# Performance work log

Measured on AMD Instinct MI355X. Metric: run time of the kernel, lower is better.

Reference implementation:

```python
import jax, jax.numpy as jnp
import numpy as np

E, H, T_MAX = 1024, 16, 2048
HS = E // H
EPS = 1e-5


def _layernorm(x, g, b):
    m = jnp.mean(x, axis=-1, keepdims=True)
    v = jnp.mean(jnp.square(x - m), axis=-1, keepdims=True)
    return (x - m) * jax.lax.rsqrt(v + EPS) * g + b


def setup_inputs() -> dict:
    key = jax.random.key(0)
    ks = jax.random.split(key, 8)
    B, T = 2, 2048
    s = 0.02
    return {
        "x": jax.random.normal(ks[0], (B, T, E), jnp.float32),
        "ln1_g": jnp.ones((E,), jnp.float32),
        "ln1_b": jnp.zeros((E,), jnp.float32),
        "Wk": jax.random.normal(ks[1], (H, E, HS), jnp.float32) * s,  # stacked per-head key weights (x @ Wk)
        "Wv": jax.random.normal(ks[2], (H, E, HS), jnp.float32) * s,
        "Wproj": jax.random.normal(ks[3], (E, E), jnp.float32) * s,
        "bproj": jnp.zeros((E,), jnp.float32),
        "ln2_g": jnp.ones((E,), jnp.float32),
        "ln2_b": jnp.zeros((E,), jnp.float32),
        "W1": jax.random.normal(ks[4], (E, 4 * E), jnp.float32) * s,
        "b1": jnp.zeros((4 * E,), jnp.float32),
        "W2": jax.random.normal(ks[5], (4 * E, E), jnp.float32) * s,
        "b2": jnp.zeros((E,), jnp.float32),
    }


def reference(x, ln1_g, ln1_b, Wk, Wv, Wproj, bproj, ln2_g, ln2_b, W1, b1, W2, b2):
    B, T, C = x.shape
    h = _layernorm(x, ln1_g, ln1_b)
    # NOTE: original code uses the KEY projection for both q and k (q = self.key(x))
    k = jnp.einsum('bte,hed->bhtd', h, Wk)
    q = k
    wei = jnp.einsum('bhtd,bhsd->bhts', q, k) * (C ** -0.5)  # scale by full n_embd, as in source
    causal = jnp.tril(jnp.ones((T, T), bool))
    wei = jnp.where(causal, wei, -jnp.inf)
    # source applies softmax over dim=1 (the query/row axis of the TxT matrix)
    wei = jax.nn.softmax(wei, axis=2)
    v = jnp.einsum('bte,hed->bhtd', h, Wv)
    attn = jnp.einsum('bhts,bhsd->bhtd', wei, v)          # [B,H,T,HS]
    attn = attn.transpose(0, 2, 1, 3).reshape(B, T, C)    # concat heads
    x = x + attn @ Wproj + bproj
    h2 = _layernorm(x, ln2_g, ln2_b)
    x = x + jax.nn.relu(h2 @ W1 + b1) @ W2 + b2
    return x
```

## Files before the change

kernel.cpp:

```cpp
#include <hip/hip_runtime.h>

using bf16x8 = __attribute__((ext_vector_type(8))) __bf16;
using f32x4  = __attribute__((ext_vector_type(4))) float;

__device__ __forceinline__ f32x4 mfma16(bf16x8 a, bf16x8 b, f32x4 c) {
  return __builtin_amdgcn_mfma_f32_16x16x32_bf16(a, b, c, 0, 0, 0);
}

__device__ __forceinline__ unsigned short f2bf(float f) {
  union { float f; unsigned int u; } x; x.f = f;
  unsigned int u = x.u + 0x7FFFu + ((x.u >> 16) & 1u);
  return (unsigned short)(u >> 16);
}

__device__ __forceinline__ unsigned int cvtpk_bf16(float lo, float hi) {
  unsigned int r;
  asm("v_cvt_pk_bf16_f32 %0, %1, %2" : "=v"(r) : "v"(lo), "v"(hi));
  return r;
}

__device__ __forceinline__ float fexp2(float x) {
#if __has_builtin(__builtin_amdgcn_exp2f)
  return __builtin_amdgcn_exp2f(x);
#else
  float r; asm("v_exp_f32 %0, %1" : "=v"(r) : "v"(x)); return r;
#endif
}

__device__ __forceinline__ void gl_lds16(const unsigned short* g, unsigned short* l) {
  __builtin_amdgcn_global_load_lds(
      (__attribute__((address_space(1))) void*)(g),
      (__attribute__((address_space(3))) void*)(l), 16, 0, 0);
}

__device__ __forceinline__ bf16x8 rdsw64(const unsigned short* base, int r, int ch) {
  int c = ch ^ (r & 7);
  return *reinterpret_cast<const bf16x8*>(base + ((size_t)r * 8 + c) * 8);
}

__global__ __launch_bounds__(256) void transpose_cvt(const float* __restrict__ in,
                                                     unsigned short* __restrict__ out,
                                                     int R, int C) {
  __shared__ float t[32][33];
  int b = blockIdx.z;
  const float* inb = in + (size_t)b * R * C;
  unsigned short* outb = out + (size_t)b * R * C;
  int tx = threadIdx.x & 31, ty = threadIdx.x >> 5;
  int c0 = blockIdx.x * 32, r0 = blockIdx.y * 32;
#pragma unroll
  for (int i = 0; i < 4; ++i)
    t[ty + i * 8][tx] = inb[(size_t)(r0 + ty + i * 8) * C + c0 + tx];
  __syncthreads();
#pragma unroll
  for (int i = 0; i < 4; ++i)
    outb[(size_t)(c0 + ty + i * 8) * R + r0 + tx] = f2bf(t[tx][ty + i * 8]);
}

__global__ __launch_bounds__(256) void ln_bf16(const float* __restrict__ x,
                                               const float* __restrict__ g,
                                               const float* __restrict__ bta,
                                               unsigned short* __restrict__ out) {
  int row = blockIdx.x, tid = threadIdx.x;
  float4 v = reinterpret_cast<const float4*>(x + (size_t)row * 1024)[tid];
  float s = v.x + v.y + v.z + v.w;
  float s2 = v.x * v.x + v.y * v.y + v.z * v.z + v.w * v.w;
#pragma unroll
  for (int m = 1; m < 64; m <<= 1) { s += __shfl_xor(s, m); s2 += __shfl_xor(s2, m); }
  __shared__ float red[8];
  int w = tid >> 6;
  if ((tid & 63) == 0) { red[w] = s; red[w + 4] = s2; }
  __syncthreads();
  s  = red[0] + red[1] + red[2] + red[3];
  s2 = red[4] + red[5] + red[6] + red[7];
  float mean = s * (1.f / 1024.f);
  float var  = s2 * (1.f / 1024.f) - mean * mean;
  float rstd = rsqrtf(var + 1e-5f);
  float4 gv = reinterpret_cast<const float4*>(g)[tid];
  float4 bv = reinterpret_cast<const float4*>(bta)[tid];
  ushort4 o;
  o.x = f2bf((v.x - mean) * rstd * gv.x + bv.x);
  o.y = f2bf((v.y - mean) * rstd * gv.y + bv.y);
  o.z = f2bf((v.z - mean) * rstd * gv.z + bv.z);
  o.w = f2bf((v.w - mean) * rstd * gv.w + bv.w);
  reinterpret_cast<ushort4*>(out + (size_t)row * 1024)[tid] = o;
}

__device__ __forceinline__ void stage_half(const unsigned short* gbase, int K,
                                           unsigned short* lds, int tid) {
#pragma unroll
  for (int j = 0; j < 2; ++j) {
    int lr = j * 64 + (tid >> 3);
    int c  = (tid & 7) ^ (lr & 7);
    gl_lds16(gbase + (size_t)lr * K + c * 8, lds + (size_t)(j * 512 + tid) * 8);
  }
}

__device__ __forceinline__ bf16x8 rdfrag(const unsigned short* base, int r, int k) {
  return *reinterpret_cast<const bf16x8*>(base + ((size_t)r * 8 + (k ^ (r & 7))) * 8);
}

__global__ __launch_bounds__(512, 2) void gemm256_relu(const unsigned short* __restrict__ A,
                                                       const unsigned short* __restrict__ Bt,
                                                       unsigned short* __restrict__ C,
                                                       const float* __restrict__ bias,
                                                       int M, int N, int K) {
  __shared__ __align__(16) unsigned short LA[2][256 * 64];
  __shared__ __align__(16) unsigned short LB[2][256 * 64];
  int tid = threadIdx.x, lane = tid & 63, w = tid >> 6;
  int l15 = lane & 15, lh = lane >> 4;
  int wr = (w >> 2) * 128, wc = (w & 3) * 64;
  int bid = blockIdx.x;
  int xcd = bid & 7, g = bid >> 3;
  int bm = (xcd >> 1) * 4 + (g >> 3);
  int bn = (xcd & 1) * 8 + (g & 7);
  const unsigned short* Ab = A + (size_t)(bm * 256) * K;
  const unsigned short* Bb = Bt + (size_t)(bn * 256) * K;
  f32x4 acc[8][4] = {};
  int NT = K >> 6;
  stage_half(Ab, K, &LA[0][0], tid);
  stage_half(Ab + (size_t)128 * K, K, &LA[0][128 * 64], tid);
  stage_half(Bb, K, &LB[0][0], tid);
  stage_half(Bb + (size_t)128 * K, K, &LB[0][128 * 64], tid);
  asm volatile("s_waitcnt vmcnt(0)" ::: "memory");
  __builtin_amdgcn_s_barrier();
  for (int t = 0; t < NT; ++t) {
    int cur = t & 1;
    const unsigned short* la = &LA[cur][0];
    const unsigned short* lb = &LB[cur][0];
    unsigned short* na = &LA[cur ^ 1][0];
    unsigned short* nb = &LB[cur ^ 1][0];
    int k0n = (t + 1) << 6;
    bool more = (t + 1 < NT);
    bf16x8 bfr[4][2];
#pragma unroll
    for (int q = 0; q < 4; ++q) {
      if (more) {
        if (q == 0)      stage_half(Ab + k0n, K, na, tid);
        else if (q == 1) stage_half(Ab + (size_t)128 * K + k0n, K, na + 128 * 64, tid);
        else if (q == 2) stage_half(Bb + k0n, K, nb, tid);
        else             stage_half(Bb + (size_t)128 * K + k0n, K, nb + 128 * 64, tid);
      }
      if (q == 0) {
        if (more) asm volatile("s_waitcnt vmcnt(2)" ::: "memory");
        else      asm volatile("s_waitcnt vmcnt(0)" ::: "memory");
        __builtin_amdgcn_s_barrier();
      }
      bf16x8 aq[2][2];
#pragma unroll
      for (int i = 0; i < 2; ++i)
#pragma unroll
        for (int kk = 0; kk < 2; ++kk)
          aq[i][kk] = rdfrag(la, wr + q * 32 + i * 16 + l15, kk * 4 + lh);
      if (q == 0) {
#pragma unroll
        for (int ni = 0; ni < 4; ++ni)
#pragma unroll
          for (int kk = 0; kk < 2; ++kk)
            bfr[ni][kk] = rdfrag(lb, wc + ni * 16 + l15, kk * 4 + lh);
      }
      if (q != 0) __builtin_amdgcn_s_barrier();
      __builtin_amdgcn_s_setprio(1);
#pragma unroll
      for (int kk = 0; kk < 2; ++kk)
#pragma unroll
        for (int i = 0; i < 2; ++i)
#pragma unroll
          for (int ni = 0; ni < 4; ++ni)
            acc[q * 2 + i][ni] = mfma16(aq[i][kk], bfr[ni][kk], acc[q * 2 + i][ni]);
      __builtin_amdgcn_s_setprio(0);
      __builtin_amdgcn_s_barrier();
    }
  }
#pragma unroll
  for (int mi = 0; mi < 8; ++mi)
#pragma unroll
    for (int ni = 0; ni < 4; ++ni) {
      int row0 = bm * 256 + wr + mi * 16 + lh * 4;
      int col  = bn * 256 + wc + ni * 16 + l15;
      float bv = bias[col];
#pragma unroll
      for (int r = 0; r < 4; ++r) {
        float v = fmaxf(acc[mi][ni][r] + bv, 0.f);
        C[(size_t)(row0 + r) * N + col] = f2bf(v);
      }
    }
}

#define GBK 128
#define KSCL 0.04508422f

__device__ __forceinline__ bf16x8 rd128(const unsigned short* base, int r, int ch) {
  int c = ch ^ ((r & 7) << 1);
  return *reinterpret_cast<const bf16x8*>(base + (size_t)r * GBK + c * 8);
}

template<int TM, int MODE>
__global__ __launch_bounds__(256) void gemm_bf16(const unsigned short* __restrict__ A,
                                                 const unsigned short* __restrict__ Bt,
                                                 void* __restrict__ Cout,
                                                 unsigned short* __restrict__ Cout2,
                                                 const float* __restrict__ bias,
                                                 const float* __restrict__ resid,
                                                 const float* __restrict__ scvec,
                                                 int M, int N, int K) {
  constexpr int MI = TM / 32;
  constexpr int AJ = TM / 16;
  __shared__ __align__(16) unsigned short Sh[(TM + 128) * GBK];
  unsigned short* As = Sh;
  unsigned short* Bs = Sh + TM * GBK;
  int tid = threadIdx.x;
  int lane = tid & 63, w = tid >> 6;
  int l15 = lane & 15, lh = lane >> 4;
  int wr = (w >> 1) * (TM / 2), wc = (w & 1) * 64;
  int nblk = N >> 7;
  int rows = M / TM;
  int bm, bn;
  if (nblk == 8 && (rows & 7) == 0) {
    int bid = blockIdx.x;
    int xcd = bid & 7, g = bid >> 3;
    bm = xcd * (rows >> 3) + (g >> 3);
    bn = g & 7;
  } else {
    bm = blockIdx.x / nblk; bn = blockIdx.x % nblk;
  }
  const unsigned short* ApJ[AJ];
  const unsigned short* BpJ[8];
#pragma unroll
  for (int j = 0; j < AJ; ++j) {
    int row = j * 16 + (tid >> 4);
    int ch  = (tid & 15) ^ ((row & 7) << 1);
    ApJ[j] = A + (size_t)(bm * TM + row) * K + ch * 8;
  }
#pragma unroll
  for (int j = 0; j < 8; ++j) {
    int row = j * 16 + (tid >> 4);
    int ch  = (tid & 15) ^ ((row & 7) << 1);
    BpJ[j] = Bt + (size_t)(bn * 128 + row) * K + ch * 8;
  }
  f32x4 acc[MI][4] = {};
  for (int k0 = 0; k0 < K; k0 += GBK) {
#pragma unroll
    for (int j = 0; j < AJ; ++j)
      gl_lds16(ApJ[j] + k0, &As[(j * 256 + tid) * 8]);
#pragma unroll
    for (int j = 0; j < 8; ++j)
      gl_lds16(BpJ[j] + k0, &Bs[(j * 256 + tid) * 8]);
    __syncthreads();
    bf16x8 af[MI][4], bfr[4][4];
#pragma unroll
    for (int i = 0; i < MI; ++i)
#pragma unroll
      for (int kk = 0; kk < 4; ++kk)
        af[i][kk] = rd128(As, wr + i * 16 + l15, kk * 4 + lh);
#pragma unroll
    for (int i = 0; i < 4; ++i)
#pragma unroll
      for (int kk = 0; kk < 4; ++kk)
        bfr[i][kk] = rd128(Bs, wc + i * 16 + l15, kk * 4 + lh);
#pragma unroll
    for (int kk = 0; kk < 4; ++kk)
#pragma unroll
      for (int mi = 0; mi < MI; ++mi)
#pragma unroll
        for (int ni = 0; ni < 4; ++ni)
          acc[mi][ni] = mfma16(af[mi][kk], bfr[ni][kk], acc[mi][ni]);
    __syncthreads();
  }
  if constexpr (MODE == 3) {
#pragma unroll
    for (int mi = 0; mi < MI; ++mi) {
#pragma unroll
      for (int ni = 0; ni < 4; ++ni) {
        int tl = wr + mi * 16 + lh * 4;
        int dl = wc + ni * 16 + l15;
        int colg = bn * 128 + dl;
        int bb = bm >> 5, hh = colg >> 6;
        const float* sp = scvec + (size_t)(bb * 16 + hh) * 2048 + (bm & 31) * 64 + tl;
        float4 rs = *reinterpret_cast<const float4*>(sp);
        unsigned int p0 = f2bf(acc[mi][ni][0] * rs.x) | ((unsigned int)f2bf(acc[mi][ni][1] * rs.y) << 16);
        unsigned int p1 = f2bf(acc[mi][ni][2] * rs.z) | ((unsigned int)f2bf(acc[mi][ni][3] * rs.w) << 16);
        uint2 pk = {p0, p1};
        *reinterpret_cast<uint2*>(&Sh[dl * 64 + (tl ^ ((dl & 7) << 3))]) = pk;
      }
    }
    __syncthreads();
    int dr = tid >> 1, th = (tid & 1) * 32;
    int bb = bm >> 5, tbase = (bm & 31) * 64;
    size_t colg = bn * 128 + dr;
    unsigned short* Vt = (unsigned short*)Cout;
#pragma unroll
    for (int j = 0; j < 4; ++j) {
      int t = th + j * 8;
      int4 v = *reinterpret_cast<const int4*>(&Sh[dr * 64 + (t ^ ((dr & 7) << 3))]);
      *reinterpret_cast<int4*>(&Vt[((size_t)bb * 1024 + colg) * 2048 + tbase + t]) = v;
    }
  } else {
#pragma unroll
    for (int mi = 0; mi < MI; ++mi) {
#pragma unroll
      for (int ni = 0; ni < 4; ++ni) {
        int row0 = bm * TM + wr + mi * 16 + lh * 4;
        int col  = bn * 128 + wc + ni * 16 + l15;
        float bv = (MODE == 2) ? 0.f : bias[col];
#pragma unroll
        for (int r = 0; r < 4; ++r) {
          int row = row0 + r;
          float v = acc[mi][ni][r] + bv;
          if constexpr (MODE == 0) {
            v += resid[(size_t)row * N + col];
            ((float*)Cout)[(size_t)row * N + col] = v;
          } else {
            ((unsigned short*)Cout)[(size_t)row * N + col] = f2bf(v);
            Cout2[(size_t)row * N + col] = f2bf(v * KSCL);
          }
        }
      }
    }
  }
}

__global__ __launch_bounds__(512) void attn_stats(const unsigned short* __restrict__ Kb,
                                                  const unsigned short* __restrict__ Kbs,
                                                  float* __restrict__ colrcp) {
  __shared__ __align__(16) unsigned short Kt[2][64 * 64];
  int bid = blockIdx.x;
  int q = bid >> 8, x = (bid >> 5) & 7, bh = bid & 31;
  int b = bh >> 4, h = bh & 15;
  int sb = q ? (15 - x) : x;
  int tid = threadIdx.x, lane = tid & 63, w = tid >> 6;
  int l15 = lane & 15, lh = lane >> 4;
  int s0 = sb * 128, sw = s0 + w * 16;
  const unsigned short* Kp  = Kb  + ((size_t)b * 2048) * 1024 + h * 64;
  const unsigned short* Kps = Kbs + ((size_t)b * 2048) * 1024 + h * 64;
  bf16x8 as[2];
#pragma unroll
  for (int kc = 0; kc < 2; ++kc)
    as[kc] = *reinterpret_cast<const bf16x8*>(Kp + (size_t)(sw + l15) * 1024 + kc * 32 + (lh << 3));
  int srow = tid >> 3;
  int sch  = (tid & 7) ^ (srow & 7);
  const unsigned short* ksrc = Kps + (size_t)srow * 1024 + sch * 8;
  gl_lds16(ksrc + (size_t)s0 * 1024, &Kt[0][tid * 8]);
  __syncthreads();
  float l[4] = {0.f, 0.f, 0.f, 0.f};
  int nt = 32 - 2 * sb;
  for (int it = 0; it < nt; ++it) {
    int t0 = s0 + it * 64;
    int cur = it & 1;
    if (it + 1 < nt)
      gl_lds16(ksrc + (size_t)(t0 + 64) * 1024, &Kt[cur ^ 1][tid * 8]);
    if (t0 + 63 >= sw) {
      bool dmask = (t0 < sw + 16);
#pragma unroll
      for (int tf = 0; tf < 4; ++tf) {
        int tr = tf * 16 + l15;
        bf16x8 bt0 = rdsw64(&Kt[cur][0], tr, lh);
        bf16x8 bt1 = rdsw64(&Kt[cur][0], tr, 4 + lh);
        f32x4 z = {};
        f32x4 sa = mfma16(as[1], bt1, mfma16(as[0], bt0, z));
        int tg = t0 + tr;
#pragma unroll
        for (int r = 0; r < 4; ++r) {
          float e = fexp2(sa[r]);
          if (dmask) { int sg = sw + lh * 4 + r; e = (tg >= sg) ? e : 0.f; }
          l[r] += e;
        }
      }
    }
    __syncthreads();
  }
#pragma unroll
  for (int m = 1; m < 16; m <<= 1)
#pragma unroll
    for (int r = 0; r < 4; ++r)
      l[r] += __shfl_xor(l[r], m);
  if (l15 == 0) {
#pragma unroll
    for (int r = 0; r < 4; ++r)
      colrcp[(size_t)bh * 2048 + sw + lh * 4 + r] = 1.f / l[r];
  }
}

__global__ __launch_bounds__(512) void attn_pv(const unsigned short* __restrict__ Kb,
                                               const unsigned short* __restrict__ Kbs,
                                               const unsigned short* __restrict__ Vt,
                                               unsigned short* __restrict__ attn) {
  __shared__ __align__(16) unsigned short Ks[2][64 * 64];
  __shared__ __align__(16) unsigned short Vs[3][64 * 64];
  __shared__ __align__(16) unsigned short Pl[8][2][16][68];
  int bid = blockIdx.x;
  int q = bid >> 8, x = (bid >> 5) & 7, bh = bid & 31;
  int b = bh >> 4, h = bh & 15;
  int tb = q ? x : (15 - x);
  int tid = threadIdx.x, lane = tid & 63, w = tid >> 6;
  int l15 = lane & 15, lh = lane >> 4;
  int t0 = tb * 128, tw = t0 + w * 16;
  const unsigned short* Kp  = Kb  + ((size_t)b * 2048) * 1024 + h * 64;
  const unsigned short* Kps = Kbs + ((size_t)b * 2048) * 1024 + h * 64;
  const unsigned short* Vp  = Vt + (size_t)bh * 64 * 2048;
  bf16x8 at[2];
#pragma unroll
  for (int kc = 0; kc < 2; ++kc)
    at[kc] = *reinterpret_cast<const bf16x8*>(Kp + (size_t)(tw + l15) * 1024 + kc * 32 + (lh << 3));
  int srow = tid >> 3;
  int sch  = (tid & 7) ^ (srow & 7);
  const unsigned short* ksrc = Kps + (size_t)srow * 1024 + sch * 8;
  const unsigned short* vsrc = Vp + (size_t)srow * 2048 + sch * 8;
  int nt = 2 * tb + 2;
  gl_lds16(ksrc, &Ks[0][tid * 8]);
  gl_lds16(vsrc, &Vs[0][tid * 8]);
  __syncthreads();
  f32x4 acc[4] = {};
  for (int it = 0; it < nt; ++it) {
    int s0 = it * 64;
    const unsigned short* ksCur = &Ks[it & 1][0];
    if (it + 1 < nt) {
      gl_lds16(ksrc + (size_t)(s0 + 64) * 1024, &Ks[(it + 1) & 1][tid * 8]);
      gl_lds16(vsrc + (s0 + 64), &Vs[(it + 1) % 3][tid * 8]);
    }
    if (s0 <= tw + 15) {
      bool dmask = (s0 + 63 > tw);
#pragma unroll
      for (int sf = 0; sf < 4; ++sf) {
        int sr = sf * 16 + l15;
        bf16x8 ks0 = rdsw64(ksCur, sr, lh);
        bf16x8 ks1 = rdsw64(ksCur, sr, 4 + lh);
        f32x4 z = {};
        f32x4 sa = mfma16(ks1, at[1], mfma16(ks0, at[0], z));
        float pe[4];
#pragma unroll
        for (int r = 0; r < 4; ++r) {
          float p = fexp2(sa[r]);
          if (dmask) {
            int sg = s0 + sf * 16 + lh * 4 + r;
            int tg = tw + l15;
            p = (sg <= tg) ? p : 0.f;
          }
          pe[r] = p;
        }
        unsigned int u0 = cvtpk_bf16(pe[0], pe[1]);
        unsigned int u1 = cvtpk_bf16(pe[2], pe[3]);
        unsigned long long pk = (unsigned long long)u0 | ((unsigned long long)u1 << 32);
        *reinterpret_cast<unsigned long long*>(&Pl[w][it & 1][l15][sf * 16 + lh * 4]) = pk;
      }
    }
    if (it > 0) {
      int pit = it - 1;
      if (pit * 64 <= tw + 15) {
        const unsigned short* vsPrev = &Vs[pit % 3][0];
#pragma unroll
        for (int c2 = 0; c2 < 2; ++c2) {
          bf16x8 pa = *reinterpret_cast<const bf16x8*>(&Pl[w][pit & 1][l15][c2 * 32 + (lh << 3)]);
#pragma unroll
          for (int nf = 0; nf < 4; ++nf) {
            int dr = nf * 16 + l15;
            bf16x8 vb = rdsw64(vsPrev, dr, c2 * 4 + lh);
            acc[nf] = mfma16(pa, vb, acc[nf]);
          }
        }
      }
    }
    __syncthreads();
  }
  {
    int pit = nt - 1;
    if (pit * 64 <= tw + 15) {
      const unsigned short* vsPrev = &Vs[pit % 3][0];
#pragma unroll
      for (int c2 = 0; c2 < 2; ++c2) {
        bf16x8 pa = *reinterpret_cast<const bf16x8*>(&Pl[w][pit & 1][l15][c2 * 32 + (lh << 3)]);
#pragma unroll
        for (int nf = 0; nf < 4; ++nf) {
          int dr = nf * 16 + l15;
          bf16x8 vb = rdsw64(vsPrev, dr, c2 * 4 + lh);
          acc[nf] = mfma16(pa, vb, acc[nf]);
        }
      }
    }
  }
#pragma unroll
  for (int nf = 0; nf < 4; ++nf)
#pragma unroll
    for (int r = 0; r < 4; ++r) {
      int t = tw + lh * 4 + r;
      attn[(size_t)(b * 2048 + t) * 1024 + h * 64 + nf * 16 + l15] = f2bf(acc[nf][r]);
    }
}

extern "C" void kernel_launch(void* const* d_in, const int* in_sizes, int n_in,
                              void* d_out, int out_size, void* d_ws, size_t ws_size,
                              hipStream_t stream) {
  (void)in_sizes; (void)n_in; (void)out_size; (void)ws_size;
  const float* x     = (const float*)d_in[0];
  const float* ln1_g = (const float*)d_in[1];
  const float* ln1_b = (const float*)d_in[2];
  const float* Wk    = (const float*)d_in[3];
  const float* Wv    = (const float*)d_in[4];
  const float* Wproj = (const float*)d_in[5];
  const float* bproj = (const float*)d_in[6];
  const float* ln2_g = (const float*)d_in[7];
  const float* ln2_b = (const float*)d_in[8];
  const float* W1    = (const float*)d_in[9];
  const float* b1    = (const float*)d_in[10];
  const float* W2    = (const float*)d_in[11];
  const float* b2    = (const float*)d_in[12];
  float* out = (float*)d_out;

  char* ws = (char*)d_ws;
  size_t off = 0;
  auto alloc = [&](size_t bytes) { void* p = ws + off; off += (bytes + 255) & ~(size_t)255; return p; };
  unsigned short* bufA = (unsigned short*)alloc((size_t)4096 * 1024 * 2);
  unsigned short* wk_t = (unsigned short*)alloc((size_t)1024 * 1024 * 2);
  unsigned short* wv_t = (unsigned short*)alloc((size_t)1024 * 1024 * 2);
  unsigned short* wp_t = (unsigned short*)alloc((size_t)1024 * 1024 * 2);
  unsigned short* w1_t = (unsigned short*)alloc((size_t)1024 * 4096 * 2);
  unsigned short* w2_t = (unsigned short*)alloc((size_t)4096 * 1024 * 2);
  unsigned short* Kb   = (unsigned short*)alloc((size_t)4096 * 1024 * 2);
  unsigned short* Kbs  = (unsigned short*)alloc((size_t)4096 * 1024 * 2);
  unsigned short* Vt   = (unsigned short*)alloc((size_t)4096 * 1024 * 2);
  float* colrcp = (float*)alloc((size_t)32 * 2048 * 4);
  float* y      = (float*)alloc((size_t)4096 * 1024 * 4);
  unsigned short* act = (unsigned short*)alloc((size_t)4096 * 4096 * 2);

  dim3 b256(256), b512(512);
  transpose_cvt<<<dim3(2, 32, 16), b256, 0, stream>>>(Wk, wk_t, 1024, 64);
  transpose_cvt<<<dim3(2, 32, 16), b256, 0, stream>>>(Wv, wv_t, 1024, 64);
  transpose_cvt<<<dim3(32, 32, 1), b256, 0, stream>>>(Wproj, wp_t, 1024, 1024);
  transpose_cvt<<<dim3(128, 32, 1), b256, 0, stream>>>(W1, w1_t, 1024, 4096);
  transpose_cvt<<<dim3(32, 128, 1), b256, 0, stream>>>(W2, w2_t, 4096, 1024);

  ln_bf16<<<4096, b256, 0, stream>>>(x, ln1_g, ln1_b, bufA);
  gemm_bf16<64, 2><<<512, b256, 0, stream>>>(bufA, wk_t, Kb, Kbs, nullptr, nullptr, nullptr, 4096, 1024, 1024);
  attn_stats<<<512, b512, 0, stream>>>(Kb, Kbs, colrcp);
  gemm_bf16<64, 3><<<512, b256, 0, stream>>>(bufA, wv_t, Vt, nullptr, nullptr, nullptr, colrcp, 4096, 1024, 1024);
  attn_pv<<<512, b512, 0, stream>>>(Kb, Kbs, Vt, bufA);
  gemm_bf16<64, 0><<<512, b256, 0, stream>>>(bufA, wp_t, y, nullptr, bproj, x, nullptr, 4096, 1024, 1024);
  ln_bf16<<<4096, b256, 0, stream>>>(y, ln2_g, ln2_b, bufA);
  gemm256_relu<<<256, dim3(512), 0, stream>>>(bufA, w1_t, act, b1, 4096, 4096, 1024);
  gemm_bf16<64, 0><<<512, b256, 0, stream>>>(act, w2_t, out, nullptr, b2, y, nullptr, 4096, 1024, 4096);
}
```

Baseline: 240.1 us.

## Double-buffer LDS in generic bf16 GEMM with BK=64 and prefetch overlap

The generic bf16 GEMM moves from a single-buffered K-tile of 128 to two LDS buffers of K=64. Loads for the next tile are issued before the MFMAs on the current tile, and a partial vmcnt wait plus raw barriers replace the full __syncthreads. The goal is to hide global-to-LDS latency behind compute. The change also raises wave priority around the MFMA block. In exchange there are twice as many loop iterations and barriers, and the kernel relies on an rdsw64 helper that is assumed to exist elsewhere.

```diff
diff --git a/kernel.cpp b/kernel.cpp
--- a/kernel.cpp
+++ b/kernel.cpp
@@ -186,13 +186,7 @@
     }
 }
 
-#define GBK 128
 #define KSCL 0.04508422f
-
-__device__ __forceinline__ bf16x8 rd128(const unsigned short* base, int r, int ch) {
-  int c = ch ^ ((r & 7) << 1);
-  return *reinterpret_cast<const bf16x8*>(base + (size_t)r * GBK + c * 8);
-}
 
 template<int TM, int MODE>
 __global__ __launch_bounds__(256) void gemm_bf16(const unsigned short* __restrict__ A,
@@ -203,11 +197,10 @@
                                                  const float* __restrict__ resid,
                                                  const float* __restrict__ scvec,
                                                  int M, int N, int K) {
-  constexpr int MI = TM / 32;
-  constexpr int AJ = TM / 16;
-  __shared__ __align__(16) unsigned short Sh[(TM + 128) * GBK];
-  unsigned short* As = Sh;
-  unsigned short* Bs = Sh + TM * GBK;
+  constexpr int MI  = TM / 32;
+  constexpr int ALD = TM / 32;
+  constexpr int NLD = ALD + 4;
+  __shared__ __align__(16) unsigned short Sh[2][(TM + 128) * 64];
   int tid = threadIdx.x;
   int lane = tid & 63, w = tid >> 6;
   int l15 = lane & 15, lh = lane >> 4;
@@ -223,49 +216,68 @@
   } else {
     bm = blockIdx.x / nblk; bn = blockIdx.x % nblk;
   }
-  const unsigned short* ApJ[AJ];
-  const unsigned short* BpJ[8];
-#pragma unroll
-  for (int j = 0; j < AJ; ++j) {
-    int row = j * 16 + (tid >> 4);
-    int ch  = (tid & 15) ^ ((row & 7) << 1);
-    ApJ[j] = A + (size_t)(bm * TM + row) * K + ch * 8;
-  }
-#pragma unroll
-  for (int j = 0; j < 8; ++j) {
-    int row = j * 16 + (tid >> 4);
-    int ch  = (tid & 15) ^ ((row & 7) << 1);
-    BpJ[j] = Bt + (size_t)(bn * 128 + row) * K + ch * 8;
+  const unsigned short* Asrc[ALD];
+  const unsigned short* Bsrc[4];
+#pragma unroll
+  for (int j = 0; j < ALD; ++j) {
+    int row = j * 32 + (tid >> 3);
+    int ch  = (tid & 7) ^ (row & 7);
+    Asrc[j] = A + (size_t)(bm * TM + row) * K + ch * 8;
+  }
+#pragma unroll
+  for (int j = 0; j < 4; ++j) {
+    int row = j * 32 + (tid >> 3);
+    int ch  = (tid & 7) ^ (row & 7);
+    Bsrc[j] = Bt + (size_t)(bn * 128 + row) * K + ch * 8;
   }
   f32x4 acc[MI][4] = {};
-  for (int k0 = 0; k0 < K; k0 += GBK) {
-#pragma unroll
-    for (int j = 0; j < AJ; ++j)
-      gl_lds16(ApJ[j] + k0, &As[(j * 256 + tid) * 8]);
-#pragma unroll
-    for (int j = 0; j < 8; ++j)
-      gl_lds16(BpJ[j] + k0, &Bs[(j * 256 + tid) * 8]);
-    __syncthreads();
-    bf16x8 af[MI][4], bfr[4][4];
+  int NT = K >> 6;
+  {
+#pragma unroll
+    for (int j = 0; j < ALD; ++j) gl_lds16(Asrc[j], &Sh[0][(j * 256 + tid) * 8]);
+#pragma unroll
+    for (int j = 0; j < 4; ++j)  gl_lds16(Bsrc[j], &Sh[0][TM * 64 + (j * 256 + tid) * 8]);
+  }
+  for (int t = 0; t < NT; ++t) {
+    int cur = t & 1;
+    const unsigned short* Asc = &Sh[cur][0];
+    const unsigned short* Bsc = &Sh[cur][TM * 64];
+    if (t + 1 < NT) {
+      int k0 = (t + 1) << 6;
+      unsigned short* Asn = &Sh[cur ^ 1][0];
+      unsigned short* Bsn = &Sh[cur ^ 1][TM * 64];
+#pragma unroll
+      for (int j = 0; j < ALD; ++j) gl_lds16(Asrc[j] + k0, Asn + (j * 256 + tid) * 8);
+#pragma unroll
+      for (int j = 0; j < 4; ++j)  gl_lds16(Bsrc[j] + k0, Bsn + (j * 256 + tid) * 8);
+      asm volatile("s_waitcnt vmcnt(%0)" :: "i"(NLD) : "memory");
+    } else {
+      asm volatile("s_waitcnt vmcnt(0)" ::: "memory");
+    }
+    __builtin_amdgcn_s_barrier();
+    bf16x8 af[MI][2], bfr[4][2];
 #pragma unroll
     for (int i = 0; i < MI; ++i)
 #pragma unroll
-      for (int kk = 0; kk < 4; ++kk)
-        af[i][kk] = rd128(As, wr + i * 16 + l15, kk * 4 + lh);
+      for (int kk = 0; kk < 2; ++kk)
+        af[i][kk] = rdsw64(Asc, wr + i * 16 + l15, kk * 4 + lh);
 #pragma unroll
     for (int i = 0; i < 4; ++i)
 #pragma unroll
-      for (int kk = 0; kk < 4; ++kk)
-        bfr[i][kk] = rd128(Bs, wc + i * 16 + l15, kk * 4 + lh);
-#pragma unroll
-    for (int kk = 0; kk < 4; ++kk)
+      for (int kk = 0; kk < 2; ++kk)
+        bfr[i][kk] = rdsw64(Bsc, wc + i * 16 + l15, kk * 4 + lh);
+    __builtin_amdgcn_s_setprio(1);
+#pragma unroll
+    for (int kk = 0; kk < 2; ++kk)
 #pragma unroll
       for (int mi = 0; mi < MI; ++mi)
 #pragma unroll
         for (int ni = 0; ni < 4; ++ni)
           acc[mi][ni] = mfma16(af[mi][kk], bfr[ni][kk], acc[mi][ni]);
-    __syncthreads();
-  }
+    __builtin_amdgcn_s_setprio(0);
+    __builtin_amdgcn_s_barrier();
+  }
+  unsigned short* Sh0 = &Sh[0][0];
   if constexpr (MODE == 3) {
 #pragma unroll
     for (int mi = 0; mi < MI; ++mi) {
@@ -280,7 +292,7 @@
         unsigned int p0 = f2bf(acc[mi][ni][0] * rs.x) | ((unsigned int)f2bf(acc[mi][ni][1] * rs.y) << 16);
         unsigned int p1 = f2bf(acc[mi][ni][2] * rs.z) | ((unsigned int)f2bf(acc[mi][ni][3] * rs.w) << 16);
         uint2 pk = {p0, p1};
-        *reinterpret_cast<uint2*>(&Sh[dl * 64 + (tl ^ ((dl & 7) << 3))]) = pk;
+        *reinterpret_cast<uint2*>(&Sh0[dl * 64 + (tl ^ ((dl & 7) << 3))]) = pk;
       }
     }
     __syncthreads();
@@ -291,7 +303,7 @@
 #pragma unroll
     for (int j = 0; j < 4; ++j) {
       int t = th + j * 8;
-      int4 v = *reinterpret_cast<const int4*>(&Sh[dr * 64 + (t ^ ((dr & 7) << 3))]);
+      int4 v = *reinterpret_cast<const int4*>(&Sh0[dr * 64 + (t ^ ((dr & 7) << 3))]);
       *reinterpret_cast<int4*>(&Vt[((size_t)bb * 1024 + colg) * 2048 + tbase + t]) = v;
     }
   } else {
```

After: 231.2 us. -3.7%, faster.
